# Performance work log

Hardware: AMD Instinct MI355X
Metric: run time of the kernel (lower is better)

The kernel has to match this reference:

```python
import jax, jax.numpy as jnp
import numpy as np

G = 4096        # graphs
NPG = 32        # nodes per graph
N = G * NPG     # total nodes
D = 256         # hidden (inv node feat) dim
SH = 256        # shared / node-MLP hidden dim
HDG = 50        # graph head dim
HDN = 3         # node head dim
NB = 2          # num branches (dataset IDs)


def setup_inputs() -> dict:
    key = jax.random.key(0)
    ks = jax.random.split(key, 8)
    s = 0.02
    return {
        "x": jax.random.normal(ks[0], (N, D), jnp.float32),
        "dataset_name": jax.random.randint(ks[1], (G,), 0, NB, jnp.int32),
        "batch": (jnp.arange(N) // NPG).astype(jnp.int32),
        "Wgs": jax.random.normal(ks[2], (NB, D, SH), jnp.float32) * s,
        "bgs": jnp.zeros((NB, SH), jnp.float32),
        "Wgh": jax.random.normal(ks[3], (NB, SH, 2 * HDG), jnp.float32) * s,
        "bgh": jnp.zeros((NB, 2 * HDG), jnp.float32),
        "Wn1": jax.random.normal(ks[4], (NB, D, SH), jnp.float32) * s,
        "bn1": jnp.zeros((NB, SH), jnp.float32),
        "Wn2": jax.random.normal(ks[5], (NB, SH, 2 * HDN), jnp.float32) * s,
        "bn2": jnp.zeros((NB, 2 * HDN), jnp.float32),
    }


def reference(x, dataset_name, batch, Wgs, bgs, Wgh, bgh, Wn1, bn1, Wn2, bn2):
    n_nodes = x.shape[0]
    n_graphs = dataset_name.shape[0]

    # ---- graph pooling (mean) : scatter-reduce nodes -> graphs ----
    counts = jax.ops.segment_sum(jnp.ones((n_nodes,), x.dtype), batch, num_segments=n_graphs)
    x_graph = jax.ops.segment_sum(x, batch, num_segments=n_graphs) / counts[:, None]  # [G, D]

    # ---- graph head: per-branch shared MLP + head, then branch dispatch ----
    hg = jax.nn.relu(jnp.einsum("gd,bds->bgs", x_graph, Wgs) + bgs[:, None, :])       # [B, G, SH]
    og = jnp.einsum("bgs,bsh->bgh", hg, Wgh) + bgh[:, None, :]                        # [B, G, 2*HDG]
    out_g = og[dataset_name, jnp.arange(n_graphs)]                                    # [G, 2*HDG]
    g_head = out_g[:, :HDG]
    g_var = out_g[:, HDG:] ** 2

    # ---- node head (mlp type): per-branch MLP on nodes, dispatch by node's graph ID ----
    node_branch = dataset_name[batch]                                                 # [N]
    hn = jax.nn.relu(jnp.einsum("nd,bds->bns", x, Wn1) + bn1[:, None, :])             # [B, N, SH]
    on = jnp.einsum("bns,bsh->bnh", hn, Wn2) + bn2[:, None, :]                        # [B, N, 2*HDN]
    out_n = on[node_branch, jnp.arange(n_nodes)]                                      # [N, 2*HDN]
    n_head = out_n[:, :HDN]
    n_var = out_n[:, HDN:] ** 2

    # (outputs, outputs_var) flattened: heads then variance heads
    return (g_head, n_head, g_var, n_var)
```

## Files before the change

kernel.cpp:

```cpp
#include <hip/hip_runtime.h>
#include <hip/hip_bf16.h>


#define G_   4096
#define NPG_ 32
#define NN_  (G_*NPG_)
#define D_   256
#define SH_  256
#define HDG_ 50
#define HDN_ 3

#define OFF_GH 0
#define OFF_NH (G_*HDG_)
#define OFF_GV (OFF_NH + NN_*HDN_)
#define OFF_NV (OFF_GV + G_*HDG_)

typedef short v8s __attribute__((ext_vector_type(8)));
typedef short v4s __attribute__((ext_vector_type(4)));
typedef float v4f __attribute__((ext_vector_type(4)));

__device__ __forceinline__ unsigned short f2bfu(float v) {
    __hip_bfloat16 b = __float2bfloat16(v);
    return *reinterpret_cast<unsigned short*>(&b);
}

#define MFMA16(a, b, c) __builtin_amdgcn_mfma_f32_16x16x32_bf16((a), (b), (c), 0, 0, 0)

__global__ __launch_bounds__(512) void node_all(const float* __restrict__ x,
                                                const int* __restrict__ dsname,
                                                const float* __restrict__ Wn1,
                                                const float* __restrict__ bn1,
                                                const float* __restrict__ Wn2,
                                                const float* __restrict__ bn2,
                                                const float* __restrict__ Wgs,
                                                const float* __restrict__ Wgh,
                                                unsigned short* __restrict__ WgsT,
                                                unsigned short* __restrict__ WghP,
                                                unsigned short* __restrict__ xg,
                                                float* __restrict__ out) {
    __shared__ __align__(16) unsigned short xs[64 * 264];
    __shared__ __align__(16) unsigned short hs[64 * 264];
    __shared__ __align__(16) float red[16 * 256];
    __shared__ int glds[32];
    __shared__ int scanS[10];
    const int t = threadIdx.x;
    const int wave = t >> 6, lane = t & 63;
    const int l15 = lane & 15, quad = lane >> 4;
    const int br = blockIdx.x & 1;
    const int bslot = blockIdx.x >> 1;

    {
        const int e0 = blockIdx.x * 768;
        #pragma unroll
        for (int i = 0; i < 2; i++) {
            const int ii = t + i * 512;
            if (ii < 768) {
                const int e = e0 + ii;
                if (e < 131072) {
                    const int np = e >> 8, d = e & 255;
                    WgsT[e] = f2bfu(Wgs[(np >> 8) * 65536 + d * 256 + (np & 255)]);
                } else {
                    const int i3 = e - 131072;
                    const int npp = i3 >> 8, k = i3 & 255;
                    const int b = npp >> 7, c = npp & 127;
                    WghP[i3] = f2bfu((c < 100) ? Wgh[b * 25600 + k * 100 + c] : 0.f);
                }
            }
        }
    }

    int pre, c0;
    {
        c0 = 0;
        #pragma unroll
        for (int k = 0; k < 8; k++) c0 += (dsname[t * 8 + k] == br) ? 1 : 0;
        pre = c0;
        #pragma unroll
        for (int d = 1; d < 64; d <<= 1) {
            const int o = __shfl_up(pre, d);
            if (lane >= d) pre += o;
        }
        if (lane == 63) scanS[wave] = pre;
    }
    __syncthreads();
    if (t == 0) {
        int s = 0;
        #pragma unroll
        for (int w = 0; w < 8; w++) { const int v = scanS[w]; scanS[w] = s; s += v; }
        scanS[8] = s;
    }
    __syncthreads();
    const int cnt = scanS[8];
    const int ntile = (cnt + 1) >> 1;
    {
        int slot = scanS[wave] + (pre - c0);
        for (int k = 0; k < 8; k++) {
            const int g = t * 8 + k;
            if (dsname[g] == br) {
                const int ti2 = slot >> 1;
                const int q = ti2 - bslot;
                if (q >= 0 && (q & 127) == 0 && (q >> 7) < 16)
                    glds[(q >> 7) * 2 + (slot & 1)] = g;
                if (slot == cnt - 1) scanS[9] = g;
                slot++;
            }
        }
    }
    __syncthreads();

    const int base_n = (wave & 1) * 128 + (wave >> 1) * 32;
    v8s B1[2][8];
    float bias1[2];
    #pragma unroll
    for (int nt = 0; nt < 2; nt++) {
        const int s = base_n + nt * 16 + l15;
        const float* wp = Wn1 + br * 65536 + s;
        #pragma unroll
        for (int kt = 0; kt < 8; kt++) {
            v8s f;
            #pragma unroll
            for (int j = 0; j < 8; j++)
                f[j] = (short)f2bfu(wp[(kt * 32 + quad * 8 + j) * 256]);
            B1[nt][kt] = f;
        }
        bias1[nt] = bn1[br * 256 + s];
    }
    v8s B2[8];
    #pragma unroll
    for (int kt = 0; kt < 8; kt++) {
        v8s f;
        #pragma unroll
        for (int j = 0; j < 8; j++) {
            const int k = kt * 32 + quad * 8 + j;
            f[j] = (l15 < 6) ? (short)f2bfu(Wn2[br * 1536 + k * 6 + l15]) : (short)0;
        }
        B2[kt] = f;
    }
    float bias2 = 0.f;
    if (l15 < 6) bias2 = bn2[br * 6 + l15];

    const int r0 = t >> 6;
    const int colb = (t & 63) * 4;

    float4 pv[8];
    int ga = 0, gb = 0;
    if (bslot < ntile) {
        ga = glds[0];
        gb = (2 * bslot + 1 < cnt) ? glds[1] : scanS[9];
        const float* xa = x + (size_t)ga * 8192 + r0 * 256 + colb;
        const float* xb = x + (size_t)gb * 8192 + r0 * 256 + colb;
        #pragma unroll
        for (int k = 0; k < 4; k++) {
            pv[k]     = *(const float4*)(xa + k * 2048);
            pv[4 + k] = *(const float4*)(xb + k * 2048);
        }
    }

    for (int ti = bslot; ti < ntile; ti += 128) {
        const int gA = ga, gB = gb;

        float4 sa = make_float4(0.f, 0.f, 0.f, 0.f);
        float4 sb = make_float4(0.f, 0.f, 0.f, 0.f);
        #pragma unroll
        for (int k = 0; k < 4; k++) {
            const float4 va = pv[k], vb = pv[4 + k];
            sa.x += va.x; sa.y += va.y; sa.z += va.z; sa.w += va.w;
            sb.x += vb.x; sb.y += vb.y; sb.z += vb.z; sb.w += vb.w;
            v4s bva, bvb;
            bva[0] = (short)f2bfu(va.x); bva[1] = (short)f2bfu(va.y);
            bva[2] = (short)f2bfu(va.z); bva[3] = (short)f2bfu(va.w);
            bvb[0] = (short)f2bfu(vb.x); bvb[1] = (short)f2bfu(vb.y);
            bvb[2] = (short)f2bfu(vb.z); bvb[3] = (short)f2bfu(vb.w);
            *(v4s*)(&xs[(r0 + 8 * k) * 264 + colb])      = bva;
            *(v4s*)(&xs[(32 + r0 + 8 * k) * 264 + colb]) = bvb;
        }
        *(float4*)(&red[r0 * 256 + colb])       = sa;
        *(float4*)(&red[(8 + r0) * 256 + colb]) = sb;

        {
            const int tn = ti + 128;
            if (tn < ntile) {
                const int ix = (tn - bslot) >> 7;
                ga = glds[ix * 2];
                gb = (2 * tn + 1 < cnt) ? glds[ix * 2 + 1] : scanS[9];
                const float* xa = x + (size_t)ga * 8192 + r0 * 256 + colb;
                const float* xb = x + (size_t)gb * 8192 + r0 * 256 + colb;
                #pragma unroll
                for (int k = 0; k < 4; k++) {
                    pv[k]     = *(const float4*)(xa + k * 2048);
                    pv[4 + k] = *(const float4*)(xb + k * 2048);
                }
            }
        }
        __syncthreads();

        {
            const int g = t >> 8, c = t & 255;
            float m = 0.f;
            #pragma unroll
            for (int r = 0; r < 8; r++) m += red[(g * 8 + r) * 256 + c];
            xg[(size_t)(g ? gB : gA) * 256 + c] = f2bfu(m * (1.0f / NPG_));
        }

        v4f acc[4][2];
        #pragma unroll
        for (int mt = 0; mt < 4; mt++)
            #pragma unroll
            for (int nt = 0; nt < 2; nt++) acc[mt][nt] = (v4f){0.f, 0.f, 0.f, 0.f};
        #pragma unroll
        for (int kt = 0; kt < 8; kt++) {
            const int ko = kt * 32 + quad * 8;
            v8s a0 = *(const v8s*)(&xs[(     l15) * 264 + ko]);
            v8s a1 = *(const v8s*)(&xs[(16 + l15) * 264 + ko]);
            v8s a2 = *(const v8s*)(&xs[(32 + l15) * 264 + ko]);
            v8s a3 = *(const v8s*)(&xs[(48 + l15) * 264 + ko]);
            #pragma unroll
            for (int nt = 0; nt < 2; nt++) {
                acc[0][nt] = MFMA16(a0, B1[nt][kt], acc[0][nt]);
                acc[1][nt] = MFMA16(a1, B1[nt][kt], acc[1][nt]);
                acc[2][nt] = MFMA16(a2, B1[nt][kt], acc[2][nt]);
                acc[3][nt] = MFMA16(a3, B1[nt][kt], acc[3][nt]);
            }
        }

        #pragma unroll
        for (int nt = 0; nt < 2; nt++) {
            const int col = base_n + nt * 16 + l15;
            #pragma unroll
            for (int mt = 0; mt < 4; mt++)
                #pragma unroll
                for (int r = 0; r < 4; r++) {
                    const int row = mt * 16 + quad * 4 + r;
                    const float v = acc[mt][nt][r] + bias1[nt];
                    hs[row * 264 + col] = f2bfu(v > 0.f ? v : 0.f);
                }
        }
        __syncthreads();

        if (wave < 4) {
            v4f a2 = (v4f){0.f, 0.f, 0.f, 0.f};
            #pragma unroll
            for (int kt = 0; kt < 8; kt++) {
                v8s av = *(const v8s*)(&hs[(wave * 16 + l15) * 264 + kt * 32 + quad * 8]);
                a2 = MFMA16(av, B2[kt], a2);
            }
            if (l15 < 6) {
                #pragma unroll
                for (int r = 0; r < 4; r++) {
                    const int row = wave * 16 + quad * 4 + r;
                    const int g = (row < 32) ? gA : gB;
                    const int n = g * NPG_ + (row & 31);
                    const float v = a2[r] + bias2;
                    if (l15 < HDN_) out[OFF_NH + n * HDN_ + l15] = v;
                    else            out[OFF_NV + n * HDN_ + (l15 - HDN_)] = v * v;
                }
            }
        }
    }
}

__global__ __launch_bounds__(256) void graph_mfma2(const unsigned short* __restrict__ xg,
                                                   const int* __restrict__ dsname,
                                                   const unsigned short* __restrict__ WgsT,
                                                   const float* __restrict__ bgs,
                                                   const unsigned short* __restrict__ WghP,
                                                   const float* __restrict__ bgh,
                                                   float* __restrict__ out) {
    __shared__ __align__(16) unsigned short xs[32 * 264];
    __shared__ int bls[32];
    const int gbase = blockIdx.x * 32;
    const int t = threadIdx.x;
    const int wave = t >> 6, lane = t & 63;
    const int l15 = lane & 15, quad = lane >> 4;
    if (t < 32) bls[t] = dsname[gbase + t];

    #pragma unroll
    for (int k = 0; k < 4; k++) {
        const int flat = k * 2048 + t * 8;
        *(v8s*)(&xs[(flat >> 8) * 264 + (flat & 255)]) =
            *(const v8s*)(xg + (size_t)gbase * 256 + flat);
    }
    __syncthreads();

    v4f acc[2][8];
    #pragma unroll
    for (int mt = 0; mt < 2; mt++)
        #pragma unroll
        for (int nt = 0; nt < 8; nt++) acc[mt][nt] = (v4f){0.f, 0.f, 0.f, 0.f};

    const unsigned short* Ab = &xs[l15 * 264 + quad * 8];
    const unsigned short* Bb = WgsT + (wave * 128 + l15) * 256 + quad * 8;

    #pragma unroll
    for (int kt = 0; kt < 8; kt++) {
        const int ko = kt * 32;
        v8s a0 = *(const v8s*)(Ab + ko);
        v8s a1 = *(const v8s*)(Ab + 16 * 264 + ko);
        #pragma unroll
        for (int nt = 0; nt < 8; nt++) {
            v8s bv = *(const v8s*)(Bb + nt * 16 * 256 + ko);
            acc[0][nt] = MFMA16(a0, bv, acc[0][nt]);
            acc[1][nt] = MFMA16(a1, bv, acc[1][nt]);
        }
    }
    __syncthreads();

    {
        const int bw = wave >> 1;
        #pragma unroll
        for (int nt = 0; nt < 8; nt++) {
            const int sp = wave * 128 + nt * 16 + l15;
            const int s_local = sp & 255;
            const float bias = bgs[sp];
            #pragma unroll
            for (int mt = 0; mt < 2; mt++)
                #pragma unroll
                for (int r = 0; r < 4; r++) {
                    const int row = mt * 16 + quad * 4 + r;
                    if (bls[row] == bw) {
                        const float v = acc[mt][nt][r] + bias;
                        xs[row * 264 + s_local] = f2bfu(v > 0.f ? v : 0.f);
                    }
                }
        }
    }
    __syncthreads();

    v4f acc2[2][4];
    #pragma unroll
    for (int mt = 0; mt < 2; mt++)
        #pragma unroll
        for (int nt = 0; nt < 4; nt++) acc2[mt][nt] = (v4f){0.f, 0.f, 0.f, 0.f};

    const unsigned short* B2 = WghP + ((wave * 4) * 16 + l15) * 256 + quad * 8;
    #pragma unroll
    for (int kt = 0; kt < 8; kt++) {
        const int ko = kt * 32;
        v8s a0 = *(const v8s*)(&xs[l15 * 264 + ko + quad * 8]);
        v8s a1 = *(const v8s*)(&xs[(16 + l15) * 264 + ko + quad * 8]);
        #pragma unroll
        for (int nt = 0; nt < 4; nt++) {
            v8s bv = *(const v8s*)(B2 + nt * 16 * 256 + ko);
            acc2[0][nt] = MFMA16(a0, bv, acc2[0][nt]);
            acc2[1][nt] = MFMA16(a1, bv, acc2[1][nt]);
        }
    }

    #pragma unroll
    for (int nt = 0; nt < 4; nt++) {
        const int npp  = (wave * 4 + nt) * 16 + l15;
        const int bo   = npp >> 7, c = npp & 127;
        if (c < 2 * HDG_) {
            const float bias = bgh[bo * 2 * HDG_ + c];
            #pragma unroll
            for (int mt = 0; mt < 2; mt++)
                #pragma unroll
                for (int r = 0; r < 4; r++) {
                    const int row = mt * 16 + quad * 4 + r;
                    if (bls[row] == bo) {
                        const float o = acc2[mt][nt][r] + bias;
                        const int g = gbase + row;
                        if (c < HDG_) out[OFF_GH + g * HDG_ + c] = o;
                        else          out[OFF_GV + g * HDG_ + (c - HDG_)] = o * o;
                    }
                }
        }
    }
}

extern "C" void kernel_launch(void* const* d_in, const int* in_sizes, int n_in,
                              void* d_out, int out_size, void* d_ws, size_t ws_size,
                              hipStream_t stream) {
    const float* x      = (const float*)d_in[0];
    const int*   dsname = (const int*)d_in[1];
    const float* Wgs = (const float*)d_in[3];
    const float* bgs = (const float*)d_in[4];
    const float* Wgh = (const float*)d_in[5];
    const float* bgh = (const float*)d_in[6];
    const float* Wn1 = (const float*)d_in[7];
    const float* bn1 = (const float*)d_in[8];
    const float* Wn2 = (const float*)d_in[9];
    const float* bn2 = (const float*)d_in[10];
    float* out = (float*)d_out;

    unsigned short* wsbuf = (unsigned short*)d_ws;
    unsigned short* WgsT  = wsbuf + 131072;
    unsigned short* WghP  = wsbuf + 262144;
    unsigned short* xg    = wsbuf + 335872;

    node_all   <<<256,     512, 0, stream>>>(x, dsname, Wn1, bn1, Wn2, bn2,
                                             Wgs, Wgh, WgsT, WghP, xg, out);
    graph_mfma2<<<G_ / 32, 256, 0, stream>>>(xg, dsname, WgsT, bgs, WghP, bgh, out);
}
```

Measured before the change: 248.9 us.

## Fuse graph head into node kernel using per-block pooled means in LDS

The second graph-head kernel and the global bf16 weight pre-conversion pass are removed. Each block keeps the mean-pooled graph features of the graphs it processed in shared memory, then loads its branch's Wgs/Wgh slices directly from fp32 and runs the two graph-head GEMMs itself. This drops one launch, the xg round trip through global memory and the separate weight-transpose stores. In exchange each block does strided fp32 weight gathers, adds LDS use and a serial tail after the node loop, and assumes at most 16 tiles per block.

```diff
diff --git a/kernel.cpp b/kernel.cpp
--- a/kernel.cpp
+++ b/kernel.cpp
@@ -26,21 +26,21 @@
 
 #define MFMA16(a, b, c) __builtin_amdgcn_mfma_f32_16x16x32_bf16((a), (b), (c), 0, 0, 0)
 
-__global__ __launch_bounds__(512) void node_all(const float* __restrict__ x,
-                                                const int* __restrict__ dsname,
-                                                const float* __restrict__ Wn1,
-                                                const float* __restrict__ bn1,
-                                                const float* __restrict__ Wn2,
-                                                const float* __restrict__ bn2,
-                                                const float* __restrict__ Wgs,
-                                                const float* __restrict__ Wgh,
-                                                unsigned short* __restrict__ WgsT,
-                                                unsigned short* __restrict__ WghP,
-                                                unsigned short* __restrict__ xg,
-                                                float* __restrict__ out) {
+__global__ __launch_bounds__(512) void fused_all(const float* __restrict__ x,
+                                                 const int* __restrict__ dsname,
+                                                 const float* __restrict__ Wn1,
+                                                 const float* __restrict__ bn1,
+                                                 const float* __restrict__ Wn2,
+                                                 const float* __restrict__ bn2,
+                                                 const float* __restrict__ Wgs,
+                                                 const float* __restrict__ bgs,
+                                                 const float* __restrict__ Wgh,
+                                                 const float* __restrict__ bgh,
+                                                 float* __restrict__ out) {
     __shared__ __align__(16) unsigned short xs[64 * 264];
     __shared__ __align__(16) unsigned short hs[64 * 264];
     __shared__ __align__(16) float red[16 * 256];
+    __shared__ __align__(16) unsigned short xgl[32 * 264];
     __shared__ int glds[32];
     __shared__ int scanS[10];
     const int t = threadIdx.x;
@@ -48,26 +48,6 @@
     const int l15 = lane & 15, quad = lane >> 4;
     const int br = blockIdx.x & 1;
     const int bslot = blockIdx.x >> 1;
-
-    {
-        const int e0 = blockIdx.x * 768;
-        #pragma unroll
-        for (int i = 0; i < 2; i++) {
-            const int ii = t + i * 512;
-            if (ii < 768) {
-                const int e = e0 + ii;
-                if (e < 131072) {
-                    const int np = e >> 8, d = e & 255;
-                    WgsT[e] = f2bfu(Wgs[(np >> 8) * 65536 + d * 256 + (np & 255)]);
-                } else {
-                    const int i3 = e - 131072;
-                    const int npp = i3 >> 8, k = i3 & 255;
-                    const int b = npp >> 7, c = npp & 127;
-                    WghP[i3] = f2bfu((c < 100) ? Wgh[b * 25600 + k * 100 + c] : 0.f);
-                }
-            }
-        }
-    }
 
     int pre, c0;
     {
@@ -158,6 +138,7 @@
 
     for (int ti = bslot; ti < ntile; ti += 128) {
         const int gA = ga, gB = gb;
+        const int lt = (ti - bslot) >> 7;
 
         float4 sa = make_float4(0.f, 0.f, 0.f, 0.f);
         float4 sb = make_float4(0.f, 0.f, 0.f, 0.f);
@@ -199,7 +180,7 @@
             float m = 0.f;
             #pragma unroll
             for (int r = 0; r < 8; r++) m += red[(g * 8 + r) * 256 + c];
-            xg[(size_t)(g ? gB : gA) * 256 + c] = f2bfu(m * (1.0f / NPG_));
+            xgl[(lt * 2 + g) * 264 + c] = f2bfu(m * (1.0f / NPG_));
         }
 
         v4f acc[4][2];
@@ -257,113 +238,95 @@
             }
         }
     }
-}
-
-__global__ __launch_bounds__(256) void graph_mfma2(const unsigned short* __restrict__ xg,
-                                                   const int* __restrict__ dsname,
-                                                   const unsigned short* __restrict__ WgsT,
-                                                   const float* __restrict__ bgs,
-                                                   const unsigned short* __restrict__ WghP,
-                                                   const float* __restrict__ bgh,
-                                                   float* __restrict__ out) {
-    __shared__ __align__(16) unsigned short xs[32 * 264];
-    __shared__ int bls[32];
-    const int gbase = blockIdx.x * 32;
-    const int t = threadIdx.x;
-    const int wave = t >> 6, lane = t & 63;
-    const int l15 = lane & 15, quad = lane >> 4;
-    if (t < 32) bls[t] = dsname[gbase + t];
-
-    #pragma unroll
-    for (int k = 0; k < 4; k++) {
-        const int flat = k * 2048 + t * 8;
-        *(v8s*)(&xs[(flat >> 8) * 264 + (flat & 255)]) =
-            *(const v8s*)(xg + (size_t)gbase * 256 + flat);
-    }
-    __syncthreads();
-
-    v4f acc[2][8];
-    #pragma unroll
-    for (int mt = 0; mt < 2; mt++)
-        #pragma unroll
-        for (int nt = 0; nt < 8; nt++) acc[mt][nt] = (v4f){0.f, 0.f, 0.f, 0.f};
-
-    const unsigned short* Ab = &xs[l15 * 264 + quad * 8];
-    const unsigned short* Bb = WgsT + (wave * 128 + l15) * 256 + quad * 8;
-
-    #pragma unroll
-    for (int kt = 0; kt < 8; kt++) {
-        const int ko = kt * 32;
-        v8s a0 = *(const v8s*)(Ab + ko);
-        v8s a1 = *(const v8s*)(Ab + 16 * 264 + ko);
-        #pragma unroll
-        for (int nt = 0; nt < 8; nt++) {
-            v8s bv = *(const v8s*)(Bb + nt * 16 * 256 + ko);
-            acc[0][nt] = MFMA16(a0, bv, acc[0][nt]);
-            acc[1][nt] = MFMA16(a1, bv, acc[1][nt]);
-        }
-    }
-    __syncthreads();
-
-    {
-        const int bw = wave >> 1;
-        #pragma unroll
-        for (int nt = 0; nt < 8; nt++) {
-            const int sp = wave * 128 + nt * 16 + l15;
-            const int s_local = sp & 255;
-            const float bias = bgs[sp];
+
+    const int ntl = (ntile > bslot) ? ((ntile - 1 - bslot) / 128 + 1) : 0;
+    const int ngr = ntl * 2;
+    if (ngr > 0) {
+        __syncthreads();
+
+        #pragma unroll
+        for (int nt = 0; nt < 2; nt++) {
+            const int s = base_n + nt * 16 + l15;
+            const float* wp = Wgs + br * 65536 + s;
+            #pragma unroll
+            for (int kt = 0; kt < 8; kt++) {
+                v8s f;
+                #pragma unroll
+                for (int j = 0; j < 8; j++)
+                    f[j] = (short)f2bfu(wp[(kt * 32 + quad * 8 + j) * 256]);
+                B1[nt][kt] = f;
+            }
+            bias1[nt] = bgs[br * 256 + s];
+        }
+        const int c2 = wave * 16 + l15;
+        #pragma unroll
+        for (int kt = 0; kt < 8; kt++) {
+            v8s f;
+            #pragma unroll
+            for (int j = 0; j < 8; j++) {
+                const int k = kt * 32 + quad * 8 + j;
+                f[j] = (c2 < 100) ? (short)f2bfu(Wgh[br * 25600 + k * 100 + c2]) : (short)0;
+            }
+            B2[kt] = f;
+        }
+        const float bias2g = (c2 < 100) ? bgh[br * 100 + c2] : 0.f;
+
+        v4f acg[2][2];
+        #pragma unroll
+        for (int mt = 0; mt < 2; mt++)
+            #pragma unroll
+            for (int nt = 0; nt < 2; nt++) acg[mt][nt] = (v4f){0.f, 0.f, 0.f, 0.f};
+        #pragma unroll
+        for (int kt = 0; kt < 8; kt++) {
+            const int ko = kt * 32 + quad * 8;
+            v8s a0 = *(const v8s*)(&xgl[(     l15) * 264 + ko]);
+            v8s a1 = *(const v8s*)(&xgl[(16 + l15) * 264 + ko]);
+            #pragma unroll
+            for (int nt = 0; nt < 2; nt++) {
+                acg[0][nt] = MFMA16(a0, B1[nt][kt], acg[0][nt]);
+                acg[1][nt] = MFMA16(a1, B1[nt][kt], acg[1][nt]);
+            }
+        }
+        #pragma unroll
+        for (int nt = 0; nt < 2; nt++) {
+            const int col = base_n + nt * 16 + l15;
             #pragma unroll
             for (int mt = 0; mt < 2; mt++)
                 #pragma unroll
                 for (int r = 0; r < 4; r++) {
                     const int row = mt * 16 + quad * 4 + r;
-                    if (bls[row] == bw) {
-                        const float v = acc[mt][nt][r] + bias;
-                        xs[row * 264 + s_local] = f2bfu(v > 0.f ? v : 0.f);
+                    const float v = acg[mt][nt][r] + bias1[nt];
+                    hs[row * 264 + col] = f2bfu(v > 0.f ? v : 0.f);
+                }
+        }
+        __syncthreads();
+
+        v4f ao0 = (v4f){0.f, 0.f, 0.f, 0.f};
+        v4f ao1 = (v4f){0.f, 0.f, 0.f, 0.f};
+        #pragma unroll
+        for (int kt = 0; kt < 8; kt++) {
+            const int ko = kt * 32 + quad * 8;
+            v8s av0 = *(const v8s*)(&hs[(     l15) * 264 + ko]);
+            v8s av1 = *(const v8s*)(&hs[(16 + l15) * 264 + ko]);
+            ao0 = MFMA16(av0, B2[kt], ao0);
+            ao1 = MFMA16(av1, B2[kt], ao1);
+        }
+        if (c2 < 2 * HDG_) {
+            #pragma unroll
+            for (int mt = 0; mt < 2; mt++) {
+                #pragma unroll
+                for (int r = 0; r < 4; r++) {
+                    const int lg = mt * 16 + quad * 4 + r;
+                    if (lg < ngr) {
+                        const int ltg = lg >> 1, p = lg & 1;
+                        const int slot = 2 * (bslot + ltg * 128) + p;
+                        const int g = (slot < cnt) ? glds[ltg * 2 + p] : scanS[9];
+                        const float o = (mt ? ao1[r] : ao0[r]) + bias2g;
+                        if (c2 < HDG_) out[OFF_GH + g * HDG_ + c2] = o;
+                        else           out[OFF_GV + g * HDG_ + (c2 - HDG_)] = o * o;
                     }
                 }
-        }
-    }
-    __syncthreads();
-
-    v4f acc2[2][4];
-    #pragma unroll
-    for (int mt = 0; mt < 2; mt++)
-        #pragma unroll
-        for (int nt = 0; nt < 4; nt++) acc2[mt][nt] = (v4f){0.f, 0.f, 0.f, 0.f};
-
-    const unsigned short* B2 = WghP + ((wave * 4) * 16 + l15) * 256 + quad * 8;
-    #pragma unroll
-    for (int kt = 0; kt < 8; kt++) {
-        const int ko = kt * 32;
-        v8s a0 = *(const v8s*)(&xs[l15 * 264 + ko + quad * 8]);
-        v8s a1 = *(const v8s*)(&xs[(16 + l15) * 264 + ko + quad * 8]);
-        #pragma unroll
-        for (int nt = 0; nt < 4; nt++) {
-            v8s bv = *(const v8s*)(B2 + nt * 16 * 256 + ko);
-            acc2[0][nt] = MFMA16(a0, bv, acc2[0][nt]);
-            acc2[1][nt] = MFMA16(a1, bv, acc2[1][nt]);
-        }
-    }
-
-    #pragma unroll
-    for (int nt = 0; nt < 4; nt++) {
-        const int npp  = (wave * 4 + nt) * 16 + l15;
-        const int bo   = npp >> 7, c = npp & 127;
-        if (c < 2 * HDG_) {
-            const float bias = bgh[bo * 2 * HDG_ + c];
-            #pragma unroll
-            for (int mt = 0; mt < 2; mt++)
-                #pragma unroll
-                for (int r = 0; r < 4; r++) {
-                    const int row = mt * 16 + quad * 4 + r;
-                    if (bls[row] == bo) {
-                        const float o = acc2[mt][nt][r] + bias;
-                        const int g = gbase + row;
-                        if (c < HDG_) out[OFF_GH + g * HDG_ + c] = o;
-                        else          out[OFF_GV + g * HDG_ + (c - HDG_)] = o * o;
-                    }
-                }
+            }
         }
     }
 }
@@ -383,12 +346,6 @@
     const float* bn2 = (const float*)d_in[10];
     float* out = (float*)d_out;
 
-    unsigned short* wsbuf = (unsigned short*)d_ws;
-    unsigned short* WgsT  = wsbuf + 131072;
-    unsigned short* WghP  = wsbuf + 262144;
-    unsigned short* xg    = wsbuf + 335872;
-
-    node_all   <<<256,     512, 0, stream>>>(x, dsname, Wn1, bn1, Wn2, bn2,
-                                             Wgs, Wgh, WgsT, WghP, xg, out);
-    graph_mfma2<<<G_ / 32, 256, 0, stream>>>(xg, dsname, WgsT, bgs, WghP, bgh, out);
+    fused_all<<<256, 512, 0, stream>>>(x, dsname, Wn1, bn1, Wn2, bn2,
+                                       Wgs, bgs, Wgh, bgh, out);
 }
```

Result: slower. 255.7 us (+2.7%).
